# Optimization experiments

Hardware: AMD Instinct MI355X
Metric: run time of the kernel (lower is better)

Reference implementation:

```python
import jax, jax.numpy as jnp
import numpy as np

VOCAB, EMBED, CONV_C, HID, LABELS = 50257, 512, 512, 1024, 128
B, S = 32, 1024

def setup_inputs() -> dict:
    key = jax.random.key(0)
    ks = jax.random.split(key, 8)
    sc = lambda d: 1.0 / np.sqrt(d)
    return {
        "token_ids": jax.random.randint(ks[0], (B, S), 0, VOCAB),
        "emb_table": jax.random.normal(ks[1], (VOCAB, EMBED), jnp.float32) * 0.02,
        "conv_w": jax.random.normal(ks[2], (CONV_C, EMBED), jnp.float32) * sc(EMBED),
        "conv_b": jnp.zeros((CONV_C,), jnp.float32),
        "dec_w1": jax.random.normal(ks[3], (CONV_C, HID), jnp.float32) * sc(CONV_C),
        "dec_b1": jnp.zeros((HID,), jnp.float32),
        "dec_w2": jax.random.normal(ks[4], (HID, LABELS), jnp.float32) * sc(HID),
        "dec_b2": jnp.zeros((LABELS,), jnp.float32),
    }

def reference(token_ids, emb_table, conv_w, conv_b, dec_w1, dec_b1, dec_w2, dec_b2):
    # Embedding lookup: [B, S, E]
    x = emb_table[token_ids]
    # DocNN encoder on a length-1 sequence = kernel-1 conv + relu (+ trivial max-over-time)
    h = jax.nn.relu(jnp.einsum('bse,ce->bsc', x, conv_w) + conv_b)  # [B,S,C]
    # MLP decoder per word
    z = jax.nn.relu(jnp.einsum('bsc,ch->bsh', h, dec_w1) + dec_b1)  # [B,S,H]
    logits = jnp.einsum('bsh,hl->bsl', z, dec_w2) + dec_b2          # [B,S,L]
    # torch.cat over dim 0 of per-word outputs -> flat [B*S, L]
    return logits.reshape(-1, logits.shape[-1])
```

## Files before the change

### kernel.cpp

```cpp
#include <hip/hip_runtime.h>

typedef __bf16 bf16;
typedef __bf16 bf16x4 __attribute__((ext_vector_type(4)));
typedef __bf16 bf16x8 __attribute__((ext_vector_type(8)));
typedef float f32x4 __attribute__((ext_vector_type(4)));

#define NROWS 32768
#define EMBED 512
#define CONV_C 512
#define HID 1024
#define LABELS 128

__device__ inline void async16(const void* g, void* l) {
  __builtin_amdgcn_global_load_lds(
      (const __attribute__((address_space(1))) void*)g,
      (__attribute__((address_space(3))) void*)l, 16, 0, 0);
}

__device__ inline int swap4(int x) { return ((x >> 2) | ((x & 3) << 2)) & 15; }
__device__ inline int bitswap02(int g) {
  return ((g & 1) << 2) | (g & 0xA) | ((g >> 2) & 1);
}

__device__ inline bf16x8 cvt8_sw(const float* row, int o0, int o1) {
  f32x4 lo = *(const f32x4*)(row + o0);
  f32x4 hi = *(const f32x4*)(row + o1);
  bf16x8 r;
  r[0] = (bf16)lo[0]; r[1] = (bf16)lo[1]; r[2] = (bf16)lo[2]; r[3] = (bf16)lo[3];
  r[4] = (bf16)hi[0]; r[5] = (bf16)hi[1]; r[6] = (bf16)hi[2]; r[7] = (bf16)hi[3];
  return r;
}


__global__ void cvt_bf16(const float* __restrict__ in, bf16* __restrict__ out, int n) {
  int i = (blockIdx.x * blockDim.x + threadIdx.x) * 4;
  if (i >= n) return;
  float4 v = *(const float4*)(in + i);
  bf16x4 o;
  o.x = (bf16)v.x; o.y = (bf16)v.y; o.z = (bf16)v.z; o.w = (bf16)v.w;
  *(bf16x4*)(out + i) = o;
}

__global__ void transpose_cvt(const float* __restrict__ in, bf16* __restrict__ out,
                              int K, int N) {
  __shared__ float t[64][65];
  int kb = blockIdx.x * 64, nb = blockIdx.y * 64;
  for (int i = threadIdx.x; i < 4096; i += 256) {
    int r = i >> 6, c = i & 63;
    t[r][c] = in[(size_t)(kb + r) * N + nb + c];
  }
  __syncthreads();
  for (int i = threadIdx.x; i < 4096; i += 256) {
    int r = i >> 6, c = i & 63;
    out[(size_t)(nb + r) * K + kb + c] = (bf16)t[c][r];
  }
}

__global__ __launch_bounds__(256) void gemm1_gather(
    const int* __restrict__ tok, const float* __restrict__ emb,
    const bf16* __restrict__ convw, const float* __restrict__ bias,
    bf16* __restrict__ out, int M, int N, int K) {
  __shared__ __attribute__((aligned(16))) float lAf[128 * 32];
  __shared__ __attribute__((aligned(16))) bf16 lB[128 * 32];
  const int tid = threadIdx.x;
  const int wave = tid >> 6, lane = tid & 63;
  const int m0 = blockIdx.x * 128, n0 = blockIdx.y * 128;
  const int wm = (wave & 1) * 64, wn = (wave >> 1) * 64;
  const int lrow = lane & 15, quad = lane >> 4;
  const int slot0 = wave * 64 + lane;

  int arow[4], acol[4];
#pragma unroll
  for (int c = 0; c < 4; ++c) {
    int s = slot0 + c * 256;
    int r = s >> 3, p = s & 7;
    arow[c] = r;
    acol[c] = (p ^ (r & 7)) * 4;
  }
  int trow[4];
#pragma unroll
  for (int c = 0; c < 4; ++c) trow[c] = tok[m0 + arow[c]];

  const f32x4 zero4 = {0.f, 0.f, 0.f, 0.f};
  f32x4 acc[4][4];
#pragma unroll
  for (int i = 0; i < 4; ++i)
#pragma unroll
    for (int j = 0; j < 4; ++j) acc[i][j] = zero4;

  for (int k0 = 0; k0 < K; k0 += 32) {
#pragma unroll
    for (int c = 0; c < 4; ++c)
      async16(emb + (size_t)trow[c] * EMBED + k0 + acol[c],
              lAf + (size_t)(wave * 64 + c * 256) * 4);
#pragma unroll
    for (int c = 0; c < 2; ++c) {
      int s = slot0 + c * 256;
      int r = s >> 2, cs = s & 3;
      async16(convw + (size_t)(n0 + r) * K + k0 + cs * 8,
              lB + (size_t)(wave * 64 + c * 256) * 8);
    }
    __syncthreads();

    bf16x8 a[4], b[4];
#pragma unroll
    for (int t = 0; t < 4; ++t) {
      int r = wm + t * 16 + lrow, sw = r & 7;
      a[t] = cvt8_sw(lAf + r * 32, ((2 * quad) ^ sw) * 4, ((2 * quad + 1) ^ sw) * 4);
      b[t] = *(const bf16x8*)(lB + (wn + t * 16 + lrow) * 32 + quad * 8);
    }
#pragma unroll
    for (int mi = 0; mi < 4; ++mi)
#pragma unroll
      for (int ni = 0; ni < 4; ++ni)
        acc[mi][ni] =
            __builtin_amdgcn_mfma_f32_16x16x32_bf16(a[mi], b[ni], acc[mi][ni], 0, 0, 0);
    __syncthreads();
  }

#pragma unroll
  for (int mi = 0; mi < 4; ++mi) {
#pragma unroll
    for (int ni = 0; ni < 4; ++ni) {
      int col = n0 + wn + ni * 16 + lrow;
      float bv = bias[col];
#pragma unroll
      for (int r = 0; r < 4; ++r) {
        int row = m0 + wm + mi * 16 + quad * 4 + r;
        float v = acc[mi][ni][r] + bv;
        v = v > 0.f ? v : 0.f;
        out[(size_t)row * N + col] = (bf16)v;
      }
    }
  }
}

__global__ __launch_bounds__(256) void gemm23_fused(
    const bf16* __restrict__ h,
    const bf16* __restrict__ w1t,
    const bf16* __restrict__ w2t,
    const float* __restrict__ b1, const float* __restrict__ b2,
    float* __restrict__ out) {
  __shared__ __attribute__((aligned(16))) bf16 lA[64 * 64];
  __shared__ __attribute__((aligned(16))) bf16 lB[128 * 64];
  __shared__ __attribute__((aligned(16))) bf16 zbuf[64 * 128];
  __shared__ __attribute__((aligned(16))) bf16 lB3[128 * 128];
  const int tid = threadIdx.x, wave = tid >> 6, lane = tid & 63;
  const int m0 = blockIdx.x * 64;
  const int wm = (wave & 1) * 32, wn = (wave >> 1) * 64;
  const int lrow = lane & 15, quad = lane >> 4;
  const int slot0 = wave * 64 + lane;
  const int sw_lrow = swap4(lrow);

  int a_r[2], a_c[2];
#pragma unroll
  for (int c = 0; c < 2; ++c) {
    int s = slot0 + c * 256;
    a_r[c] = s >> 3;
    a_c[c] = ((s & 7) ^ (a_r[c] & 7)) * 8;
  }
  int b_r[4], b_c[4];
#pragma unroll
  for (int c = 0; c < 4; ++c) {
    int s = slot0 + c * 256;
    b_r[c] = s >> 3;
    b_c[c] = ((s & 7) ^ (b_r[c] & 7)) * 8;
  }
  int w2_r[8], w2_c[8];
#pragma unroll
  for (int c = 0; c < 8; ++c) {
    int s = slot0 + c * 256;
    w2_r[c] = s >> 4;
    w2_c[c] = bitswap02((s & 15) ^ swap4(w2_r[c] & 15)) * 8;
  }

  const f32x4 zero4 = {0.f, 0.f, 0.f, 0.f};
  f32x4 out_acc[2][4];
#pragma unroll
  for (int i = 0; i < 2; ++i)
#pragma unroll
    for (int j = 0; j < 4; ++j) out_acc[i][j] = zero4;

  for (int chunk = 0; chunk < 8; ++chunk) {
    f32x4 z_acc[2][4];
#pragma unroll
    for (int i = 0; i < 2; ++i)
#pragma unroll
      for (int j = 0; j < 4; ++j) z_acc[i][j] = zero4;

    const bf16* wB = w1t + (size_t)(chunk * 128) * 512;
    for (int k0 = 0; k0 < 512; k0 += 64) {
#pragma unroll
      for (int c = 0; c < 2; ++c)
        async16(h + (size_t)(m0 + a_r[c]) * 512 + k0 + a_c[c],
                lA + (size_t)(wave * 64 + c * 256) * 8);
#pragma unroll
      for (int c = 0; c < 4; ++c)
        async16(wB + (size_t)b_r[c] * 512 + k0 + b_c[c],
                lB + (size_t)(wave * 64 + c * 256) * 8);
      __syncthreads();

#pragma unroll
      for (int ks = 0; ks < 2; ++ks) {
        bf16x8 a[2], b[4];
#pragma unroll
        for (int t = 0; t < 2; ++t) {
          int row = wm + t * 16 + lrow;
          int pos = (ks * 4 + quad) ^ (row & 7);
          a[t] = *(const bf16x8*)(lA + row * 64 + pos * 8);
        }
#pragma unroll
        for (int t = 0; t < 4; ++t) {
          int row = wn + t * 16 + lrow;
          int pos = (ks * 4 + quad) ^ (row & 7);
          b[t] = *(const bf16x8*)(lB + row * 64 + pos * 8);
        }
#pragma unroll
        for (int mi = 0; mi < 2; ++mi)
#pragma unroll
          for (int ni = 0; ni < 4; ++ni)
            z_acc[mi][ni] =
                __builtin_amdgcn_mfma_f32_16x16x32_bf16(a[mi], b[ni], z_acc[mi][ni], 0, 0, 0);
      }
      __syncthreads();
    }

#pragma unroll
    for (int c = 0; c < 8; ++c)
      async16(w2t + (size_t)w2_r[c] * HID + chunk * 128 + w2_c[c],
              lB3 + (size_t)(wave * 64 + c * 256) * 8);

#pragma unroll
    for (int mi = 0; mi < 2; ++mi) {
#pragma unroll
      for (int ni = 0; ni < 4; ++ni) {
        int col = wn + ni * 16 + lrow;
        float bv = b1[chunk * 128 + col];
        int gsw = bitswap02(col >> 3);
#pragma unroll
        for (int r = 0; r < 4; ++r) {
          int row = wm + mi * 16 + quad * 4 + r;
          float v = z_acc[mi][ni][r] + bv;
          v = v > 0.f ? v : 0.f;
          int pos = gsw ^ (quad | (r << 2));
          zbuf[row * 128 + pos * 8 + (col & 7)] = (bf16)v;
        }
      }
    }
    __syncthreads();

#pragma unroll
    for (int ks = 0; ks < 4; ++ks) {
      int possw = bitswap02(ks * 4 + quad) ^ sw_lrow;
      bf16x8 a3[2], b3[4];
#pragma unroll
      for (int mi = 0; mi < 2; ++mi) {
        int row = wm + mi * 16 + lrow;
        a3[mi] = *(const bf16x8*)(zbuf + row * 128 + possw * 8);
      }
#pragma unroll
      for (int ni = 0; ni < 4; ++ni) {
        int row = wn + ni * 16 + lrow;
        b3[ni] = *(const bf16x8*)(lB3 + row * 128 + possw * 8);
      }
#pragma unroll
      for (int mi = 0; mi < 2; ++mi)
#pragma unroll
        for (int ni = 0; ni < 4; ++ni)
          out_acc[mi][ni] =
              __builtin_amdgcn_mfma_f32_16x16x32_bf16(a3[mi], b3[ni], out_acc[mi][ni], 0, 0, 0);
    }
    __syncthreads();
  }

#pragma unroll
  for (int mi = 0; mi < 2; ++mi) {
#pragma unroll
    for (int ni = 0; ni < 4; ++ni) {
      int col = wn + ni * 16 + lrow;
      float bv = b2[col];
#pragma unroll
      for (int r = 0; r < 4; ++r) {
        int row = m0 + wm + mi * 16 + quad * 4 + r;
        out[(size_t)row * LABELS + col] = out_acc[mi][ni][r] + bv;
      }
    }
  }
}


extern "C" void kernel_launch(void* const* d_in, const int* in_sizes, int n_in,
                              void* d_out, int out_size, void* d_ws, size_t ws_size,
                              hipStream_t stream) {
  const int* tok = (const int*)d_in[0];
  const float* emb = (const float*)d_in[1];
  const float* conv_w = (const float*)d_in[2];
  const float* conv_b = (const float*)d_in[3];
  const float* w1 = (const float*)d_in[4];
  const float* b1 = (const float*)d_in[5];
  const float* w2 = (const float*)d_in[6];
  const float* b2 = (const float*)d_in[7];
  float* out = (float*)d_out;

  char* ws = (char*)d_ws;
  bf16* wtc = (bf16*)(ws);
  bf16* wt1 = (bf16*)(ws + (1u << 19));
  bf16* wt2 = (bf16*)(ws + 3 * (1u << 19));
  bf16* h = (bf16*)(ws + (2u << 20));

  hipLaunchKernelGGL(cvt_bf16, dim3(256), dim3(256), 0, stream,
                     conv_w, wtc, CONV_C * EMBED);
  hipLaunchKernelGGL(transpose_cvt, dim3(8, 16), dim3(256), 0, stream,
                     w1, wt1, CONV_C, HID);
  hipLaunchKernelGGL(transpose_cvt, dim3(16, 2), dim3(256), 0, stream,
                     w2, wt2, HID, LABELS);

  hipLaunchKernelGGL(gemm1_gather, dim3(NROWS / 128, CONV_C / 128), dim3(256),
                     0, stream, tok, emb, wtc, conv_b, h, NROWS, CONV_C, EMBED);
  hipLaunchKernelGGL(gemm23_fused, dim3(NROWS / 64), dim3(256),
                     0, stream, h, wt1, wt2, b1, b2, out);
}
```

Baseline: 261.5 us.

## Double-buffer LDS tiles in both GEMM kernels to overlap loads with MFMA

Both kernels now use a ping-pong pair of LDS buffers. The next K-slice's async global-to-LDS loads are issued right after the barrier, so they overlap the MFMA work on the current slice, and one of the two barriers per iteration is dropped. In the fused decoder kernel the W2 tile prefetch is also moved ahead of the hidden-layer K loop, and zbuf now aliases the staging region. The cost is a larger shared-memory footprint (48KB and 80KB per block), which may lower how many blocks fit on each CU, plus aliasing that depends on barrier placement for correctness.

```diff
diff --git a/kernel.cpp b/kernel.cpp
--- a/kernel.cpp
+++ b/kernel.cpp
@@ -60,8 +60,7 @@
     const int* __restrict__ tok, const float* __restrict__ emb,
     const bf16* __restrict__ convw, const float* __restrict__ bias,
     bf16* __restrict__ out, int M, int N, int K) {
-  __shared__ __attribute__((aligned(16))) float lAf[128 * 32];
-  __shared__ __attribute__((aligned(16))) bf16 lB[128 * 32];
+  __shared__ __attribute__((aligned(16))) char smem[49152];
   const int tid = threadIdx.x;
   const int wave = tid >> 6, lane = tid & 63;
   const int m0 = blockIdx.x * 128, n0 = blockIdx.y * 128;
@@ -88,7 +87,9 @@
 #pragma unroll
     for (int j = 0; j < 4; ++j) acc[i][j] = zero4;
 
-  for (int k0 = 0; k0 < K; k0 += 32) {
+  auto stage = [&](int p, int k0) {
+    float* lAf = (float*)(smem + p * 24576);
+    bf16* lB = (bf16*)(smem + p * 24576 + 16384);
 #pragma unroll
     for (int c = 0; c < 4; ++c)
       async16(emb + (size_t)trow[c] * EMBED + k0 + acol[c],
@@ -100,7 +101,15 @@
       async16(convw + (size_t)(n0 + r) * K + k0 + cs * 8,
               lB + (size_t)(wave * 64 + c * 256) * 8);
     }
+  };
+
+  stage(0, 0);
+  int cur = 0;
+  for (int it = 0; it < 16; ++it) {
     __syncthreads();
+    if (it < 15) stage(cur ^ 1, (it + 1) * 32);
+    const float* lAf = (const float*)(smem + cur * 24576);
+    const bf16* lB = (const bf16*)(smem + cur * 24576 + 16384);
 
     bf16x8 a[4], b[4];
 #pragma unroll
@@ -115,7 +124,7 @@
       for (int ni = 0; ni < 4; ++ni)
         acc[mi][ni] =
             __builtin_amdgcn_mfma_f32_16x16x32_bf16(a[mi], b[ni], acc[mi][ni], 0, 0, 0);
-    __syncthreads();
+    cur ^= 1;
   }
 
 #pragma unroll
@@ -141,10 +150,9 @@
     const bf16* __restrict__ w2t,
     const float* __restrict__ b1, const float* __restrict__ b2,
     float* __restrict__ out) {
-  __shared__ __attribute__((aligned(16))) bf16 lA[64 * 64];
-  __shared__ __attribute__((aligned(16))) bf16 lB[128 * 64];
-  __shared__ __attribute__((aligned(16))) bf16 zbuf[64 * 128];
-  __shared__ __attribute__((aligned(16))) bf16 lB3[128 * 128];
+  __shared__ __attribute__((aligned(16))) char smem[81920];
+  bf16* zbuf = (bf16*)smem;
+  bf16* lB3 = (bf16*)(smem + 49152);
   const int tid = threadIdx.x, wave = tid >> 6, lane = tid & 63;
   const int m0 = blockIdx.x * 64;
   const int wm = (wave & 1) * 32, wn = (wave >> 1) * 64;
@@ -174,6 +182,19 @@
     w2_c[c] = bitswap02((s & 15) ^ swap4(w2_r[c] & 15)) * 8;
   }
 
+  auto stage = [&](int p, const bf16* wB, int k0) {
+    bf16* lA = (bf16*)(smem + p * 24576);
+    bf16* lB = (bf16*)(smem + p * 24576 + 8192);
+#pragma unroll
+    for (int c = 0; c < 2; ++c)
+      async16(h + (size_t)(m0 + a_r[c]) * 512 + k0 + a_c[c],
+              lA + (size_t)(wave * 64 + c * 256) * 8);
+#pragma unroll
+    for (int c = 0; c < 4; ++c)
+      async16(wB + (size_t)b_r[c] * 512 + k0 + b_c[c],
+              lB + (size_t)(wave * 64 + c * 256) * 8);
+  };
+
   const f32x4 zero4 = {0.f, 0.f, 0.f, 0.f};
   f32x4 out_acc[2][4];
 #pragma unroll
@@ -189,16 +210,19 @@
       for (int j = 0; j < 4; ++j) z_acc[i][j] = zero4;
 
     const bf16* wB = w1t + (size_t)(chunk * 128) * 512;
-    for (int k0 = 0; k0 < 512; k0 += 64) {
-#pragma unroll
-      for (int c = 0; c < 2; ++c)
-        async16(h + (size_t)(m0 + a_r[c]) * 512 + k0 + a_c[c],
-                lA + (size_t)(wave * 64 + c * 256) * 8);
-#pragma unroll
-      for (int c = 0; c < 4; ++c)
-        async16(wB + (size_t)b_r[c] * 512 + k0 + b_c[c],
-                lB + (size_t)(wave * 64 + c * 256) * 8);
+
+#pragma unroll
+    for (int c = 0; c < 8; ++c)
+      async16(w2t + (size_t)w2_r[c] * HID + chunk * 128 + w2_c[c],
+              lB3 + (size_t)(wave * 64 + c * 256) * 8);
+    stage(0, wB, 0);
+
+    int cur = 0;
+    for (int it = 0; it < 8; ++it) {
       __syncthreads();
+      if (it < 7) stage(cur ^ 1, wB, (it + 1) * 64);
+      const bf16* lA = (const bf16*)(smem + cur * 24576);
+      const bf16* lB = (const bf16*)(smem + cur * 24576 + 8192);
 
 #pragma unroll
       for (int ks = 0; ks < 2; ++ks) {
@@ -222,14 +246,8 @@
             z_acc[mi][ni] =
                 __builtin_amdgcn_mfma_f32_16x16x32_bf16(a[mi], b[ni], z_acc[mi][ni], 0, 0, 0);
       }
-      __syncthreads();
-    }
-
-#pragma unroll
-    for (int c = 0; c < 8; ++c)
-      async16(w2t + (size_t)w2_r[c] * HID + chunk * 128 + w2_c[c],
-              lB3 + (size_t)(wave * 64 + c * 256) * 8);
-
+      cur ^= 1;
+    }
 #pragma unroll
     for (int mi = 0; mi < 2; ++mi) {
 #pragma unroll
```

Measured after the change: 254.8 us. -2.5%, faster.
